# Kernel optimization log

Measured on AMD Instinct MI355X. Metric: run time of the kernel, lower is better.

Reference implementation:

```python
import jax, jax.numpy as jnp
import numpy as np

B, D, L = 8, 512, 2000          # batch, encoder_out_dim, seq_len
E = 300                          # embedding_dim
N1, N2 = 118, 8929               # hierarchy level sizes


def setup_inputs() -> dict:
    key = jax.random.key(0)
    k = jax.random.split(key, 6)
    H = jax.random.normal(k[0], (B, D, L), dtype=jnp.float32)
    Q1w = jax.random.normal(k[1], (N1, E), dtype=jnp.float32) * 0.05   # cat_embedding_matrix
    Q2w = jax.random.normal(k[2], (N2, E), dtype=jnp.float32) * 0.05   # label_embedding_matrix
    # Q12: xavier_uniform over [N2, N1]
    bound = float(np.sqrt(6.0 / (N1 + N2)))
    Q12w = jax.random.uniform(k[3], (N2, N1), minval=-bound, maxval=bound, dtype=jnp.float32)
    # 1x1 conv mapping: weight [D, E], bias [D] (kernel_size=1 squeezed)
    cbound = float(np.sqrt(1.0 / E))
    Wmap = jax.random.uniform(k[4], (D, E), minval=-cbound, maxval=cbound, dtype=jnp.float32)
    bmap = jax.random.uniform(k[5], (D,), minval=-cbound, maxval=cbound, dtype=jnp.float32)
    return {"H": H, "Q1w": Q1w, "Q2w": Q2w, "Q12w": Q12w, "Wmap": Wmap, "bmap": bmap}


def reference(H, Q1w, Q2w, Q12w, Wmap, bmap):
    # 1x1 conv mapping == affine map over embedding dim: [n, E] @ [E, D] + b
    Q1 = Q1w @ Wmap.T + bmap                      # [N1, D]
    E1 = jnp.einsum('nd,bdl->bnl', Q1, H)         # level-1 scores [B, N1, L]
    A1 = jax.nn.softmax(E1, axis=2)
    C1 = jnp.einsum('bnl,bdl->bnd', A1, H)        # [B, N1, D]
    C1 = jnp.einsum('mn,bnd->bmd', Q12w, C1)      # project to level 2: [B, N2, D]
    Q2 = (Q2w @ Wmap.T + bmap) * C1               # [N2, D] * [B, N2, D]
    E2 = jnp.einsum('bmd,bdl->bml', Q2, H)        # level-2 scores [B, N2, L]
    A2 = jax.nn.softmax(E2, axis=2)
    C2 = jnp.einsum('bml,bdl->bmd', A2, H)        # [B, N2, D]
    return (C2, A2)
```

## Files before the change

kernel.cpp:

```cpp
#include <hip/hip_runtime.h>

typedef short    bf16x8 __attribute__((ext_vector_type(8)));
typedef float    f32x4  __attribute__((ext_vector_type(4)));
typedef unsigned short u16x8 __attribute__((ext_vector_type(8)));

__device__ __forceinline__ unsigned short f2bf(float f) {
    unsigned u = __float_as_uint(f);
    return (unsigned short)((u + 0x7fffu + ((u >> 16) & 1u)) >> 16);
}
__device__ __forceinline__ float bf2f(unsigned short h) {
    return __uint_as_float((unsigned)h << 16);
}

template<bool> struct otype            { using T = float; };
template<>     struct otype<true>      { using T = unsigned short; };

template<int BM,int BN,int TM,int TN,bool BT,bool VA,bool VB,bool OB>
__launch_bounds__(256)
__global__ void gemm_f32(const float* __restrict__ A, int lda, long long sA,
                         const float* __restrict__ B, int ldb, long long sB,
                         void* __restrict__ Cv, int ldc, long long sC,
                         int M, int N, int K,
                         const float* __restrict__ bias,
                         const float* __restrict__ mul, int mulld)
{
    constexpr int BK  = 16;
    constexpr int GSA = BM*4/TM;
    constexpr int GSB = BN*4/TN;
    __shared__ float As[BK][BM+4];
    __shared__ float Bs[BK][BN+4];

    const int bz = blockIdx.z;
    A += (long long)bz * sA;
    B += (long long)bz * sB;
    using OT = typename otype<OB>::T;
    OT* C = (OT*)Cv + (long long)bz * sC;
    const int m0 = blockIdx.y * BM;
    const int n0 = blockIdx.x * BN;
    const int tid = threadIdx.x;
    const int tm = tid >> 4;
    const int tn = tid & 15;

    float acc[TM][TN];
#pragma unroll
    for (int i=0;i<TM;++i)
#pragma unroll
        for (int j=0;j<TN;++j) acc[i][j]=0.f;

    for (int k0=0;k0<K;k0+=BK) {
        if constexpr (VA) {
#pragma unroll
            for (int r=0;r<BM*BK/1024;++r) {
                int v = tid + r*256;
                int m = v >> 2, k4 = (v & 3)*4;
                int gm = m0+m, gk = k0+k4;
                float4 val = make_float4(0.f,0.f,0.f,0.f);
                if (gm < M) {
                    if (gk+3 < K) {
                        val = *reinterpret_cast<const float4*>(A + (long long)gm*lda + gk);
                    } else {
                        float t0 = (gk   < K) ? A[(long long)gm*lda+gk  ] : 0.f;
                        float t1 = (gk+1 < K) ? A[(long long)gm*lda+gk+1] : 0.f;
                        float t2 = (gk+2 < K) ? A[(long long)gm*lda+gk+2] : 0.f;
                        val = make_float4(t0,t1,t2,0.f);
                    }
                }
                As[k4+0][m]=val.x; As[k4+1][m]=val.y; As[k4+2][m]=val.z; As[k4+3][m]=val.w;
            }
        } else {
#pragma unroll
            for (int r=0;r<BM*BK/256;++r) {
                int e = tid + r*256;
                int m = e >> 4, k = e & 15;
                int gm=m0+m, gk=k0+k;
                As[k][m] = (gm<M && gk<K) ? A[(long long)gm*lda+gk] : 0.f;
            }
        }
        if constexpr (!BT) {
            if constexpr (VB) {
#pragma unroll
                for (int r=0;r<BK*BN/1024;++r) {
                    int v = tid + r*256;
                    int k = v / (BN/4), n4 = (v % (BN/4))*4;
                    int gk=k0+k, gn=n0+n4;
                    float4 val = make_float4(0.f,0.f,0.f,0.f);
                    if (gk < K) {
                        if (gn+3 < N) {
                            val = *reinterpret_cast<const float4*>(B + (long long)gk*ldb + gn);
                        } else {
                            float t0=(gn  <N)?B[(long long)gk*ldb+gn  ]:0.f;
                            float t1=(gn+1<N)?B[(long long)gk*ldb+gn+1]:0.f;
                            float t2=(gn+2<N)?B[(long long)gk*ldb+gn+2]:0.f;
                            val = make_float4(t0,t1,t2,0.f);
                        }
                    }
                    Bs[k][n4+0]=val.x; Bs[k][n4+1]=val.y; Bs[k][n4+2]=val.z; Bs[k][n4+3]=val.w;
                }
            } else {
#pragma unroll
                for (int r=0;r<BK*BN/256;++r) {
                    int e = tid + r*256;
                    int k = e / BN, n = e % BN;
                    int gk=k0+k, gn=n0+n;
                    Bs[k][n] = (gk<K && gn<N) ? B[(long long)gk*ldb+gn] : 0.f;
                }
            }
        } else {
            if constexpr (VB) {
#pragma unroll
                for (int r=0;r<BN*BK/1024;++r) {
                    int v = tid + r*256;
                    int n = v >> 2, k4 = (v&3)*4;
                    int gn=n0+n, gk=k0+k4;
                    float4 val = make_float4(0.f,0.f,0.f,0.f);
                    if (gn < N) {
                        if (gk+3 < K) {
                            val = *reinterpret_cast<const float4*>(B + (long long)gn*ldb + gk);
                        } else {
                            float t0=(gk  <K)?B[(long long)gn*ldb+gk  ]:0.f;
                            float t1=(gk+1<K)?B[(long long)gn*ldb+gk+1]:0.f;
                            float t2=(gk+2<K)?B[(long long)gn*ldb+gk+2]:0.f;
                            val=make_float4(t0,t1,t2,0.f);
                        }
                    }
                    Bs[k4+0][n]=val.x; Bs[k4+1][n]=val.y; Bs[k4+2][n]=val.z; Bs[k4+3][n]=val.w;
                }
            } else {
#pragma unroll
                for (int r=0;r<BN*BK/256;++r) {
                    int e = tid + r*256;
                    int n = e >> 4, k = e & 15;
                    int gn=n0+n, gk=k0+k;
                    Bs[k][n] = (gn<N && gk<K) ? B[(long long)gn*ldb+gk] : 0.f;
                }
            }
        }
        __syncthreads();
#pragma unroll
        for (int kk=0;kk<BK;++kk) {
            float a[TM], bb[TN];
#pragma unroll
            for (int g=0;g<TM/4;++g) {
                float4 t = *reinterpret_cast<const float4*>(&As[kk][g*GSA + tm*4]);
                a[4*g+0]=t.x; a[4*g+1]=t.y; a[4*g+2]=t.z; a[4*g+3]=t.w;
            }
#pragma unroll
            for (int g=0;g<TN/4;++g) {
                float4 t = *reinterpret_cast<const float4*>(&Bs[kk][g*GSB + tn*4]);
                bb[4*g+0]=t.x; bb[4*g+1]=t.y; bb[4*g+2]=t.z; bb[4*g+3]=t.w;
            }
#pragma unroll
            for (int i=0;i<TM;++i)
#pragma unroll
                for (int j=0;j<TN;++j)
                    acc[i][j] = fmaf(a[i], bb[j], acc[i][j]);
        }
        __syncthreads();
    }
#pragma unroll
    for (int i=0;i<TM;++i) {
        int row = m0 + (i>>2)*GSA + tm*4 + (i&3);
        if (row < M) {
#pragma unroll
            for (int j=0;j<TN;++j) {
                int col = n0 + (j>>2)*GSB + tn*4 + (j&3);
                if (col < N) {
                    float val = acc[i][j];
                    if (bias) val += bias[col];
                    if (mul)  val *= mul[(long long)row*mulld + col];
                    if constexpr (OB) C[(long long)row*ldc + col] = f2bf(val);
                    else              C[(long long)row*ldc + col] = val;
                }
            }
        }
    }
}

template<unsigned F>
__launch_bounds__(512, 4)
__global__ void gemm_mfma_p(const unsigned short* __restrict__ A, int lda, long long sA,
                            const unsigned short* __restrict__ Bt, int ldb, long long sB,
                            void* __restrict__ Cv, int ldc, long long sC,
                            int M, int Ncols, int NX, int NY, int NT,
                            const float* __restrict__ bias,
                            const float* __restrict__ mul, int ldm,
                            float* __restrict__ partial, long long pstride,
                            const float* __restrict__ hsum,
                            const float* __restrict__ invs,
                            float* __restrict__ a2out,
                            float* __restrict__ dump)
{
    __shared__ unsigned short lds[3][12288];

    const int nwg = gridDim.x;
    const int q = nwg >> 3, r = nwg & 7;
    const int xcd = blockIdx.x & 7, idx = blockIdx.x >> 3;
    const int wg = (xcd < r ? xcd*(q+1) : r*(q+1) + (xcd-r)*q) + idx;
    const int nx = wg % NX;
    const int t1 = wg / NX;
    const int my = t1 % NY;
    const int bz = t1 / NY;

    const int tid  = threadIdx.x;
    const int lane = tid & 63, wid = tid >> 6;
    const int wr = wid >> 2, wc = wid & 3;
    const int fr = lane & 15, fq = lane >> 4;
    const int m0 = my * 128;
    const int n0 = nx * 256;

    A  += (long long)bz * sA;
    Bt += (long long)bz * sB;

    const int srow = tid >> 2;
    const int scz  = (tid & 3) ^ ((srow >> 1) & 3);
    long long arow = m0 + srow; if (arow > M-1) arow = M-1;
    const unsigned short* aSrc  = A  + arow*lda + scz*8;
    const unsigned short* bSrc0 = Bt + (long long)(n0 + srow)*ldb + scz*8;
    const unsigned short* bSrc1 = bSrc0 + 128ll*ldb;

    bool wrblk = false, a2ok = false;
    float invv = 0.f;
    float* a2p = nullptr;
    if constexpr ((F & 64) != 0) {
        wrblk = (nx == 0);
        if (wrblk) {
            const int rrow = m0 + srow;
            a2ok = rrow < M;
            const long long ridx = (long long)bz*M + (a2ok ? rrow : M-1);
            invv = invs[ridx];
            asm volatile("" : "+v"(invv));
            a2p = a2out + ridx*2000ll;
        }
    }

    int aoff[4], boff[4];
#pragma unroll
    for (int m=0;m<4;++m) {
        const int ra = wr*64 + m*16 + fr;
        aoff[m] = ra*64 + ((fq ^ ((ra>>1)&3))*16);
    }
#pragma unroll
    for (int n=0;n<4;++n) {
        const int rb = wc*64 + n*16 + fr;
        boff[n] = 8192 + rb*64 + ((fq ^ ((rb>>1)&3))*16);
    }

    f32x4 acc[4][4];
#pragma unroll
    for (int i=0;i<4;++i)
#pragma unroll
        for (int j=0;j<4;++j) acc[i][j] = (f32x4)(0.f);

    auto stage = [&](int s, int t) {
        const int koff = t*32;
        char* base = (char*)&lds[s][0];
        __builtin_amdgcn_global_load_lds(
            (const __attribute__((address_space(1))) void*)(aSrc + koff),
            (__attribute__((address_space(3))) void*)(base + tid*16), 16, 0, 0);
        __builtin_amdgcn_global_load_lds(
            (const __attribute__((address_space(1))) void*)(bSrc0 + koff),
            (__attribute__((address_space(3))) void*)(base + 8192 + tid*16), 16, 0, 0);
        __builtin_amdgcn_global_load_lds(
            (const __attribute__((address_space(1))) void*)(bSrc1 + koff),
            (__attribute__((address_space(3))) void*)(base + 16384 + tid*16), 16, 0, 0);
    };

    stage(0, 0);
    stage(1, NT > 1 ? 1 : 0);
    asm volatile("s_waitcnt vmcnt(3)" ::: "memory");
    __builtin_amdgcn_s_barrier();

    int cur = 0, stg = 2;
    for (int kt = 0; kt < NT; ++kt) {
        int tnx = kt + 2; if (tnx > NT-1) tnx = NT-1;
        stage(stg, tnx);
        const char* bp = (const char*)&lds[cur][0];
        bf16x8 a[4], b[4];
#pragma unroll
        for (int m=0;m<4;++m) a[m] = *(const bf16x8*)(bp + aoff[m]);
#pragma unroll
        for (int n=0;n<4;++n) b[n] = *(const bf16x8*)(bp + boff[n]);
        __builtin_amdgcn_s_setprio(1);
#pragma unroll
        for (int m=0;m<4;++m)
#pragma unroll
            for (int n=0;n<4;++n)
                acc[m][n] = __builtin_amdgcn_mfma_f32_16x16x32_bf16(a[m], b[n], acc[m][n], 0, 0, 0);
        __builtin_amdgcn_s_setprio(0);
        if constexpr ((F & 64) != 0) {
            if (wrblk) {
                u16x8 av = *(const u16x8*)(bp + (tid << 4));
                const int col0 = kt*32 + scz*8;
                const bool ok = a2ok && (col0 < 2000);
                float* p0 = ok ? (a2p + col0) : (dump + (tid << 3));
                float4 o0, o1;
                o0.x = fmaf(bf2f((unsigned short)av[0]), invv, invv);
                o0.y = fmaf(bf2f((unsigned short)av[1]), invv, invv);
                o0.z = fmaf(bf2f((unsigned short)av[2]), invv, invv);
                o0.w = fmaf(bf2f((unsigned short)av[3]), invv, invv);
                o1.x = fmaf(bf2f((unsigned short)av[4]), invv, invv);
                o1.y = fmaf(bf2f((unsigned short)av[5]), invv, invv);
                o1.z = fmaf(bf2f((unsigned short)av[6]), invv, invv);
                o1.w = fmaf(bf2f((unsigned short)av[7]), invv, invv);
                *(float4*)(p0    ) = o0;
                *(float4*)(p0 + 4) = o1;
            }
        }
        asm volatile("s_waitcnt lgkmcnt(0)" ::: "memory");
        if constexpr ((F & 64) != 0) {
            if (wrblk) asm volatile("s_waitcnt vmcnt(5)" ::: "memory");
            else       asm volatile("s_waitcnt vmcnt(3)" ::: "memory");
        } else {
            asm volatile("s_waitcnt vmcnt(3)" ::: "memory");
        }
        __builtin_amdgcn_s_barrier();
        cur = (cur == 2) ? 0 : cur + 1;
        stg = (stg == 2) ? 0 : stg + 1;
    }

    if constexpr ((F & 16) != 0) {
        asm volatile("s_waitcnt vmcnt(0)" ::: "memory");
        __builtin_amdgcn_s_barrier();
        unsigned short* ep = (unsigned short*)&lds[0][0];
        unsigned short* Cb = (unsigned short*)Cv + (long long)bz * sC;
#pragma unroll
        for (int m=0;m<4;++m) {
            const int rl = wr*64 + m*16 + fq*4;
#pragma unroll
            for (int n=0;n<4;++n) {
                const int cl = wc*64 + n*16 + fr;
                const int cb = cl*2;
#pragma unroll
                for (int j=0;j<4;++j) {
                    const int row = rl + j;
                    float x = __expf(acc[m][n][j]) - 1.0f;
                    const int ch = (cb>>5) ^ ((row>>2)&3);
                    *(unsigned short*)((char*)ep + row*512 + (ch<<5) + (cb&31)) = f2bf(x);
                }
            }
        }
        __syncthreads();
        const int rq = tid >> 3;
        const int cq = tid & 7;
#pragma unroll
        for (int half=0; half<2; ++half) {
            const int row = rq + half*64;
            const int grow = m0 + row;
            float s = 0.f;
#pragma unroll
            for (int win=0; win<4; ++win) {
                const int cb = cq*16 + win*128;
                const int ch = (cb>>5) ^ ((row>>2)&3);
                u16x8 v = *(const u16x8*)((const char*)ep + row*512 + (ch<<5) + (cb&31));
#pragma unroll
                for (int i=0;i<8;++i) s += bf2f((unsigned short)v[i]);
                if (grow < M) *(u16x8*)(Cb + (long long)grow*ldc + n0 + (cb>>1)) = v;
            }
            s += __shfl_xor(s, 1); s += __shfl_xor(s, 2); s += __shfl_xor(s, 4);
            if (cq == 0 && grow < M)
                partial[(long long)nx*pstride + (long long)bz*M + grow] = s;
        }
    } else if constexpr ((F & 8) != 0) {
        unsigned short* Ct = (unsigned short*)Cv + (long long)bz * sC;
#pragma unroll
        for (int m=0;m<4;++m) {
            const int rb = m0 + wr*64 + m*16 + fq*4;
#pragma unroll
            for (int n=0;n<4;++n) {
                const int col = n0 + wc*64 + n*16 + fr;
                if (col < Ncols) {
                    float hv = 0.f;
                    if constexpr ((F & 32) != 0) hv = hsum[(long long)bz*Ncols + col];
#pragma unroll
                    for (int j=0;j<4;++j) {
                        const int row = rb + j;
                        float val = 0.f;
                        if (row < M) {
                            val = acc[m][n][j];
                            if constexpr ((F & 32) != 0) val = (val + hv) * invs[(long long)bz*M + row];
                        }
                        Ct[(long long)col*ldc + row] = f2bf(val);
                    }
                }
            }
        }
    } else if constexpr ((F & 4) != 0) {
        asm volatile("s_waitcnt vmcnt(0)" ::: "memory");
        __builtin_amdgcn_s_barrier();
        unsigned short* ep = (unsigned short*)&lds[0][0];
        unsigned short* Cb = (unsigned short*)Cv + (long long)bz * sC;
#pragma unroll
        for (int m=0;m<4;++m) {
            const int rl = wr*64 + m*16 + fq*4;
#pragma unroll
            for (int n=0;n<4;++n) {
                const int cl = wc*64 + n*16 + fr;
                const int gcol = n0 + cl;
                const int cb = cl*2;
                float bv = 0.f;
                if constexpr ((F & 1) != 0) bv = bias[gcol];
#pragma unroll
                for (int j=0;j<4;++j) {
                    const int row = rl + j;
                    float val = acc[m][n][j];
                    if constexpr ((F & 1) != 0) val += bv;
                    if constexpr ((F & 128) != 0) {
                        int mr = m0 + row; if (mr > M-1) mr = M-1;
                        val *= bf2f(((const unsigned short*)mul)[(long long)mr*ldm + gcol]);
                    }
                    if constexpr ((F & 2) != 0) {
                        int mr = m0 + row; if (mr > M-1) mr = M-1;
                        val *= mul[(long long)mr*ldm + gcol];
                    }
                    const int ch = (cb>>5) ^ ((row>>2)&3);
                    *(unsigned short*)((char*)ep + row*512 + (ch<<5) + (cb&31)) = f2bf(val);
                }
            }
        }
        __syncthreads();
        const int rq = tid >> 3;
        const int cq = tid & 7;
#pragma unroll
        for (int half=0; half<2; ++half) {
            const int row = rq + half*64;
            const int grow = m0 + row;
#pragma unroll
            for (int win=0; win<4; ++win) {
                const int cb = cq*16 + win*128;
                const int ch = (cb>>5) ^ ((row>>2)&3);
                u16x8 v = *(const u16x8*)((const char*)ep + row*512 + (ch<<5) + (cb&31));
                const int gc = n0 + (cb>>1);
                if (grow < M && gc < Ncols) *(u16x8*)(Cb + (long long)grow*ldc + gc) = v;
            }
        }
    } else {
        float* Cf = (float*)Cv + (long long)bz * sC;
#pragma unroll
        for (int m=0;m<4;++m) {
            const int rb = m0 + wr*64 + m*16 + fq*4;
#pragma unroll
            for (int n=0;n<4;++n) {
                const int col = n0 + wc*64 + n*16 + fr;
                if (col < Ncols) {
                    float bv = 0.f, hv = 0.f;
                    if constexpr ((F & 1) != 0) bv = bias[col];
                    if constexpr ((F & 32) != 0) hv = hsum[(long long)bz*Ncols + col];
#pragma unroll
                    for (int j=0;j<4;++j) {
                        const int row = rb + j;
                        if (row < M) {
                            float val = acc[m][n][j];
                            if constexpr ((F & 1)   != 0) val += bv;
                            if constexpr ((F & 2)   != 0) val *= mul[(long long)row*ldm + col];
                            if constexpr ((F & 128) != 0) val *= bf2f(((const unsigned short*)mul)[(long long)row*ldm + col]);
                            if constexpr ((F & 32)  != 0) val = (val + hv) * invs[(long long)bz*M + row];
                            Cf[(long long)row*ldc + col] = val;
                        }
                    }
                }
            }
        }
    }
}

template<bool AF32>
__launch_bounds__(512, 2)
__global__ void gemm_mfma(const void* __restrict__ Ain, int lda, long long sA,
                          const unsigned short* __restrict__ Bt, int ldb, long long sB,
                          float* __restrict__ C, int ldc, long long sC,
                          int M, int N, int K, int NT)
{
    __shared__ unsigned short As[2][128*32];
    __shared__ unsigned short Bs[2][256*32];

    const int tid  = threadIdx.x;
    const int lane = tid & 63, wid = tid >> 6;
    const int wr = wid >> 2, wc = wid & 3;
    const int fr = lane & 15, fq = lane >> 4;
    const int bz = blockIdx.z;
    const int m0 = blockIdx.y * 128;
    const int n0 = blockIdx.x * 256;

    const unsigned short* Ab = nullptr;
    const float*          Af = nullptr;
    if constexpr (AF32) Af = (const float*)Ain + (long long)bz * sA;
    else                Ab = (const unsigned short*)Ain + (long long)bz * sA;
    Bt += (long long)bz * sB;
    C  += (long long)bz * sC;

    const int srow = tid >> 2;
    const int sc   = tid & 3;
    const int scz  = sc ^ ((srow >> 1) & 3);
    int arow = m0 + srow; if (arow > M-1) arow = M-1;
    const bool am_ok = (m0 + srow) < M;
    const long long brow0 = n0 + srow;
    const long long brow1 = n0 + 128 + srow;
    const int ldsA  = wid << 10;
    const int ldsB0 = wid << 10;
    const int ldsB1 = 8192 + (wid << 10);

    f32x4 acc[4][4];
#pragma unroll
    for (int i=0;i<4;++i)
#pragma unroll
        for (int j=0;j<4;++j) acc[i][j] = (f32x4)(0.f);

    auto stage = [&](int buf, int t) {
        const long long koff = (long long)t * 32;
        __builtin_amdgcn_global_load_lds(
            (const __attribute__((address_space(1))) void*)(Bt + brow0*ldb + koff + scz*8),
            (__attribute__((address_space(3))) void*)((char*)&Bs[buf][0] + ldsB0), 16, 0, 0);
        __builtin_amdgcn_global_load_lds(
            (const __attribute__((address_space(1))) void*)(Bt + brow1*ldb + koff + scz*8),
            (__attribute__((address_space(3))) void*)((char*)&Bs[buf][0] + ldsB1), 16, 0, 0);
        if constexpr (!AF32) {
            __builtin_amdgcn_global_load_lds(
                (const __attribute__((address_space(1))) void*)(Ab + (long long)arow*lda + koff + scz*8),
                (__attribute__((address_space(3))) void*)((char*)&As[buf][0] + ldsA), 16, 0, 0);
        } else {
            const float* src = Af + (long long)arow*lda + koff + scz*8;
            const int kk = t*32 + scz*8;
            float4 z = make_float4(0.f,0.f,0.f,0.f);
            float4 v0 = (am_ok && kk   < K) ? *(const float4*)(src  ) : z;
            float4 v1 = (am_ok && kk+4 < K) ? *(const float4*)(src+4) : z;
            u16x8 o;
            o[0]=f2bf(v0.x); o[1]=f2bf(v0.y); o[2]=f2bf(v0.z); o[3]=f2bf(v0.w);
            o[4]=f2bf(v1.x); o[5]=f2bf(v1.y); o[6]=f2bf(v1.z); o[7]=f2bf(v1.w);
            *(u16x8*)((char*)&As[buf][0] + tid*16) = o;
        }
    };

    stage(0, 0);
    int cur = 0;
    for (int t = 0; t < NT; ++t) {
        __syncthreads();
        if (t + 1 < NT) stage(cur ^ 1, t + 1);
        const unsigned short* as = As[cur];
        const unsigned short* bs = Bs[cur];
        bf16x8 a[4], b[4];
#pragma unroll
        for (int m=0;m<4;++m) {
            const int ra = wr*64 + m*16 + fr;
            a[m] = *(const bf16x8*)(as + ra*32 + (fq ^ ((ra>>1)&3))*8);
        }
#pragma unroll
        for (int n=0;n<4;++n) {
            const int rb = wc*64 + n*16 + fr;
            b[n] = *(const bf16x8*)(bs + rb*32 + (fq ^ ((rb>>1)&3))*8);
        }
        __builtin_amdgcn_s_setprio(1);
#pragma unroll
        for (int m=0;m<4;++m)
#pragma unroll
            for (int n=0;n<4;++n)
                acc[m][n] = __builtin_amdgcn_mfma_f32_16x16x32_bf16(a[m], b[n], acc[m][n], 0, 0, 0);
        __builtin_amdgcn_s_setprio(0);
        cur ^= 1;
    }
#pragma unroll
    for (int m=0;m<4;++m) {
        const int rb = m0 + wr*64 + m*16 + fq*4;
#pragma unroll
        for (int n=0;n<4;++n) {
            const int col = n0 + wc*64 + n*16 + fr;
            if (col < N) {
#pragma unroll
                for (int j=0;j<4;++j) {
                    const int row = rb + j;
                    if (row < M) C[(long long)row*ldc + col] = acc[m][n][j];
                }
            }
        }
    }
}

__global__ __launch_bounds__(256) void mega_prep(const float* __restrict__ H,
                                                 unsigned short* __restrict__ Hb,
                                                 unsigned short* __restrict__ Htb,
                                                 float* __restrict__ hpart,
                                                 const float* __restrict__ Wmap,  unsigned short* __restrict__ Wb,
                                                 const float* __restrict__ Q1w,   unsigned short* __restrict__ Q1wb,
                                                 const float* __restrict__ Q2w,   unsigned short* __restrict__ Q2wb,
                                                 const float* __restrict__ Q12w,  unsigned short* __restrict__ Q12wb)
{
    __shared__ unsigned short T[64][80];
    const int tid = threadIdx.x;
    int id = blockIdx.x;
    if (id < 2048) {
        const int lt = id & 31;
        const int dt = (id >> 5) & 7;
        const int bz = id >> 8;
        const int d0 = dt * 64;
        const int l0 = lt * 64;
        const float* Hsrc = H + ((long long)bz*512 + d0) * 2000;
        const int dl = tid >> 2;
        const int lc = (tid & 3) * 16;
        float4 v[4];
        float s = 0.f;
#pragma unroll
        for (int i=0;i<4;++i) {
            const int gl = l0 + lc + i*4;
            v[i] = make_float4(0.f,0.f,0.f,0.f);
            if (gl < 2000) v[i] = *(const float4*)(Hsrc + (long long)dl*2000 + gl);
            s += (v[i].x + v[i].y) + (v[i].z + v[i].w);
            T[lc+i*4+0][dl] = f2bf(v[i].x);
            T[lc+i*4+1][dl] = f2bf(v[i].y);
            T[lc+i*4+2][dl] = f2bf(v[i].z);
            T[lc+i*4+3][dl] = f2bf(v[i].w);
        }
        {
            unsigned short* hb = Hb + ((long long)bz*512 + d0 + dl)*2048 + l0 + lc;
            u16x8 h0, h1;
            h0[0]=f2bf(v[0].x); h0[1]=f2bf(v[0].y); h0[2]=f2bf(v[0].z); h0[3]=f2bf(v[0].w);
            h0[4]=f2bf(v[1].x); h0[5]=f2bf(v[1].y); h0[6]=f2bf(v[1].z); h0[7]=f2bf(v[1].w);
            h1[0]=f2bf(v[2].x); h1[1]=f2bf(v[2].y); h1[2]=f2bf(v[2].z); h1[3]=f2bf(v[2].w);
            h1[4]=f2bf(v[3].x); h1[5]=f2bf(v[3].y); h1[6]=f2bf(v[3].z); h1[7]=f2bf(v[3].w);
            *(u16x8*)(hb    ) = h0;
            *(u16x8*)(hb + 8) = h1;
        }
        s += __shfl_xor(s, 1);
        s += __shfl_xor(s, 2);
        if ((tid & 3) == 0)
            hpart[(long long)lt*4096 + bz*512 + d0 + dl] = s;
        __syncthreads();
        unsigned short* Hdst = Htb + ((long long)bz*2048 + l0) * 512 + d0;
        const int ll = tid >> 2;
        const int dc = (tid & 3) * 16;
        u16x8 w0 = *(const u16x8*)&T[ll][dc];
        u16x8 w1 = *(const u16x8*)&T[ll][dc+8];
        *(u16x8*)(Hdst + (long long)ll*512 + dc    ) = w0;
        *(u16x8*)(Hdst + (long long)ll*512 + dc + 8) = w1;
        return;
    }
    id -= 2048;
    if (id < 640) {
        const int i = id*256 + tid;
        if (i < 512*320) {
            const int r2 = i/320, c = i - r2*320;
            Wb[i] = (c < 300) ? f2bf(Wmap[r2*300 + c]) : (unsigned short)0;
        }
    } else if (id < 788) {
        const int i = (id-640)*256 + tid;
        if (i < 118*320) {
            const int r2 = i/320, c = i - r2*320;
            Q1wb[i] = (c < 300) ? f2bf(Q1w[r2*300 + c]) : (unsigned short)0;
        }
    } else if (id < 11950) {
        const int i = (id-788)*256 + tid;
        if (i < 8929*320) {
            const int r2 = i/320, c = i - r2*320;
            Q2wb[i] = (c < 300) ? f2bf(Q2w[r2*300 + c]) : (unsigned short)0;
        }
    } else {
        const int i = (id-11950)*256 + tid;
        if (i < 8929*128) {
            const int r2 = i >> 7, c = i & 127;
            Q12wb[i] = (c < 118) ? f2bf(Q12w[r2*118 + c]) : (unsigned short)0;
        }
    }
}

__global__ __launch_bounds__(256) void reduce_hsum(const float* __restrict__ hpart,
                                                   float* __restrict__ Hsum)
{
    const int r = blockIdx.x*256 + threadIdx.x;
    float s = 0.f;
#pragma unroll
    for (int i=0;i<32;++i) s += hpart[(long long)i*4096 + r];
    Hsum[r] = s;
}

__global__ __launch_bounds__(256) void invs_k(const float* __restrict__ partial,
                                              long long pstride,
                                              float* __restrict__ invs, int n)
{
    const int r = blockIdx.x*256 + threadIdx.x;
    if (r < n) {
        float s = 0.f;
#pragma unroll
        for (int i=0;i<8;++i) s += partial[i*pstride + r];
        invs[r] = 1.0f / (2000.0f + s);
    }
}

__global__ __launch_bounds__(256) void cvt_pad_bf16(const float* __restrict__ H,
                                                    unsigned short* __restrict__ Hb)
{
    const long long idx = (long long)blockIdx.x * 256 + threadIdx.x;
    const long long row = idx >> 8;
    const int l0 = (int)(idx & 255) * 8;
    u16x8 o = (u16x8)(unsigned short)0;
    if (l0 + 8 <= 2000) {
        const float* s = H + row*2000 + l0;
        float4 v0 = *(const float4*)(s);
        float4 v1 = *(const float4*)(s+4);
        o[0]=f2bf(v0.x); o[1]=f2bf(v0.y); o[2]=f2bf(v0.z); o[3]=f2bf(v0.w);
        o[4]=f2bf(v1.x); o[5]=f2bf(v1.y); o[6]=f2bf(v1.z); o[7]=f2bf(v1.w);
    }
    *(u16x8*)(Hb + row*2048 + l0) = o;
}

__global__ __launch_bounds__(256) void cvt_transpose_bf16(const float* __restrict__ H,
                                                          unsigned short* __restrict__ Ht)
{
    __shared__ unsigned short T[64][80];
    const int bz = blockIdx.z;
    const int d0 = blockIdx.y * 64;
    const int l0 = blockIdx.x * 64;
    const float* Hsrc = H + ((long long)bz*512 + d0) * 2000;
    unsigned short* Hdst = Ht + ((long long)bz*2048 + l0) * 512 + d0;
    const int tid = threadIdx.x;
    const int dl = tid >> 2;
    const int lc = (tid & 3) * 16;
#pragma unroll
    for (int i=0;i<4;++i) {
        const int l = lc + i*4;
        const int gl = l0 + l;
        float4 v = make_float4(0.f,0.f,0.f,0.f);
        if (gl < 2000) v = *(const float4*)(Hsrc + (long long)dl*2000 + gl);
        T[l+0][dl] = f2bf(v.x);
        T[l+1][dl] = f2bf(v.y);
        T[l+2][dl] = f2bf(v.z);
        T[l+3][dl] = f2bf(v.w);
    }
    __syncthreads();
    const int ll = tid >> 2;
    const int dc = (tid & 3) * 16;
    u16x8 w0 = *(const u16x8*)&T[ll][dc];
    u16x8 w1 = *(const u16x8*)&T[ll][dc+8];
    *(u16x8*)(Hdst + (long long)ll*512 + dc    ) = w0;
    *(u16x8*)(Hdst + (long long)ll*512 + dc + 8) = w1;
}

__global__ __launch_bounds__(256) void softmax_rows(float* __restrict__ X, int L,
                                                    unsigned short* __restrict__ Xb, int Lb)
{
    const long long row = blockIdx.x;
    float* x = X + row * (long long)L;
    const int tid = threadIdx.x;
    const int nv = L >> 2;
    const bool h0 = tid < nv;
    const bool h1 = tid + 256 < nv;
    float4 t0 = make_float4(0.f,0.f,0.f,0.f);
    float4 t1 = make_float4(0.f,0.f,0.f,0.f);
    float mx = -3.402823e38f;
    if (h0) { t0 = *reinterpret_cast<const float4*>(x + 4*tid);
              mx = fmaxf(fmaxf(t0.x,t0.y), fmaxf(t0.z,t0.w)); }
    if (h1) { t1 = *reinterpret_cast<const float4*>(x + 4*(tid+256));
              mx = fmaxf(mx, fmaxf(fmaxf(t1.x,t1.y), fmaxf(t1.z,t1.w))); }
    __shared__ float sred[4];
#pragma unroll
    for (int o=32;o;o>>=1) mx = fmaxf(mx, __shfl_xor(mx, o));
    if ((tid & 63)==0) sred[tid>>6] = mx;
    __syncthreads();
    mx = fmaxf(fmaxf(sred[0],sred[1]), fmaxf(sred[2],sred[3]));
    __syncthreads();
    float s = 0.f;
    if (h0) {
        t0.x=__expf(t0.x-mx); t0.y=__expf(t0.y-mx); t0.z=__expf(t0.z-mx); t0.w=__expf(t0.w-mx);
        s += (t0.x+t0.y)+(t0.z+t0.w);
    }
    if (h1) {
        t1.x=__expf(t1.x-mx); t1.y=__expf(t1.y-mx); t1.z=__expf(t1.z-mx); t1.w=__expf(t1.w-mx);
        s += (t1.x+t1.y)+(t1.z+t1.w);
    }
#pragma unroll
    for (int o=32;o;o>>=1) s += __shfl_xor(s, o);
    if ((tid & 63)==0) sred[tid>>6] = s;
    __syncthreads();
    s = (sred[0]+sred[1])+(sred[2]+sred[3]);
    const float inv = 1.0f / s;
    if (h0) { t0.x*=inv; t0.y*=inv; t0.z*=inv; t0.w*=inv;
              *reinterpret_cast<float4*>(x + 4*tid) = t0; }
    if (h1) { t1.x*=inv; t1.y*=inv; t1.z*=inv; t1.w*=inv;
              *reinterpret_cast<float4*>(x + 4*(tid+256)) = t1; }
    if (Xb) {
        unsigned short* xb = Xb + row * (long long)Lb;
        if (h0) {
            ushort4 o; o.x=f2bf(t0.x); o.y=f2bf(t0.y); o.z=f2bf(t0.z); o.w=f2bf(t0.w);
            *reinterpret_cast<ushort4*>(xb + 4*tid) = o;
        }
        if (h1) {
            ushort4 o; o.x=f2bf(t1.x); o.y=f2bf(t1.y); o.z=f2bf(t1.z); o.w=f2bf(t1.w);
            *reinterpret_cast<ushort4*>(xb + 4*(tid+256)) = o;
        }
        if (tid < (Lb - L)/4) {
            ushort4 z; z.x=z.y=z.z=z.w=0;
            *reinterpret_cast<ushort4*>(xb + L + 4*tid) = z;
        }
    }
}

extern "C" void kernel_launch(void* const* d_in, const int* in_sizes, int n_in,
                              void* d_out, int out_size, void* d_ws, size_t ws_size,
                              hipStream_t stream)
{
    const float* H    = (const float*)d_in[0];
    const float* Q1w  = (const float*)d_in[1];
    const float* Q2w  = (const float*)d_in[2];
    const float* Q12w = (const float*)d_in[3];
    const float* Wmap = (const float*)d_in[4];
    const float* bmap = (const float*)d_in[5];

    constexpr long long B=8, D=512, L=2000, N1=118, N2=8929;
    constexpr long long C2E = B*N2*D;
    float* out = (float*)d_out;
    float* C2  = out;
    float* A2  = out + C2E;

    dim3 blk(256);

    size_t off = 0;
    auto alloc = [&](size_t n)->size_t { off = (off + 255) & ~(size_t)255; size_t o = off; off += n; return o; };
    const size_t oHb    = alloc(8ll*512*2048*2);
    const size_t oHtb   = alloc(8ll*2048*512*2);
    const size_t oWb    = alloc(512ll*320*2);
    const size_t oQ1wb  = alloc(118ll*320*2);
    const size_t oQ2wb  = alloc(8929ll*320*2);
    const size_t oQ12wb = alloc(8929ll*128*2);
    const size_t oQ1b   = alloc(118ll*512*2);
    const size_t oEmbb  = alloc(8929ll*512*2);
    const size_t oE1x   = alloc(8ll*128*2048*2);
    const size_t oC1tb  = alloc(8ll*512*128*2);
    const size_t oQ2b   = alloc(8ll*8929*512*2);
    const size_t oA2b   = alloc(8ll*8929*2048*2);
    const size_t oPart  = alloc(8ll*8*8929*4);
    const size_t oPart1 = alloc(8ll*944*4);
    const size_t oInvs  = alloc(8ll*8929*4);
    const size_t oInvs1 = alloc(944ll*4);
    const size_t oHsum  = alloc(8ll*512*4);
    const size_t oHpart = alloc(32ll*4096*4);
    const size_t FULL_NEED = off;

    char* ws = (char*)d_ws;

    if (ws_size >= FULL_NEED) {
        unsigned short* Hb    = (unsigned short*)(ws + oHb);
        unsigned short* Htb   = (unsigned short*)(ws + oHtb);
        unsigned short* Wb    = (unsigned short*)(ws + oWb);
        unsigned short* Q1wb  = (unsigned short*)(ws + oQ1wb);
        unsigned short* Q2wb  = (unsigned short*)(ws + oQ2wb);
        unsigned short* Q12wb = (unsigned short*)(ws + oQ12wb);
        unsigned short* Q1b   = (unsigned short*)(ws + oQ1b);
        unsigned short* Embb  = (unsigned short*)(ws + oEmbb);
        unsigned short* E1x   = (unsigned short*)(ws + oE1x);
        unsigned short* C1tb  = (unsigned short*)(ws + oC1tb);
        unsigned short* Q2b   = (unsigned short*)(ws + oQ2b);
        unsigned short* A2b   = (unsigned short*)(ws + oA2b);
        float*          part  = (float*)(ws + oPart);
        float*          part1 = (float*)(ws + oPart1);
        float*          invs  = (float*)(ws + oInvs);
        float*          invs1 = (float*)(ws + oInvs1);
        float*          Hsum  = (float*)(ws + oHsum);
        float*          hpart = (float*)(ws + oHpart);

        mega_prep<<<dim3(18464), blk, 0, stream>>>(H, Hb, Htb, hpart,
                                                   Wmap, Wb, Q1w, Q1wb, Q2w, Q2wb, Q12w, Q12wb);
        reduce_hsum<<<dim3(16), blk, 0, stream>>>(hpart, Hsum);

        gemm_mfma_p<5><<<dim3(2), dim3(512), 0, stream>>>(
            Q1wb, 320, 0, Wb, 320, 0, Q1b, 512, 0, 118, 512, 2, 1, 10,
            bmap, nullptr, 0, nullptr, 0, nullptr, nullptr, nullptr, nullptr);
        gemm_mfma_p<5><<<dim3(140), dim3(512), 0, stream>>>(
            Q2wb, 320, 0, Wb, 320, 0, Embb, 512, 0, 8929, 512, 2, 70, 10,
            bmap, nullptr, 0, nullptr, 0, nullptr, nullptr, nullptr, nullptr);
        gemm_mfma_p<16><<<dim3(64), dim3(512), 0, stream>>>(
            Q1b, 512, 0, Htb, 512, 2048*512, E1x, 2048, 128*2048, 118, 2048, 8, 1, 16,
            nullptr, nullptr, 0, part1, 944, nullptr, nullptr, nullptr, nullptr);
        invs_k<<<dim3(4), blk, 0, stream>>>(part1, 944, invs1, 944);
        gemm_mfma_p<40><<<dim3(16), dim3(512), 0, stream>>>(
            E1x, 2048, 128*2048, Hb, 2048, 512*2048, C1tb, 128, 512*128, 118, 512, 2, 1, 64,
            nullptr, nullptr, 0, nullptr, 0, Hsum, invs1, nullptr, nullptr);
        gemm_mfma_p<132><<<dim3(1120), dim3(512), 0, stream>>>(
            Q12wb, 128, 0, C1tb, 128, 512*128, Q2b, 512, N2*D, 8929, 512, 2, 70, 4,
            nullptr, (const float*)Embb, 512, nullptr, 0, nullptr, nullptr, nullptr, nullptr);
        gemm_mfma_p<16><<<dim3(4480), dim3(512), 0, stream>>>(
            Q2b, 512, N2*D, Htb, 512, 2048*512, A2b, 2048, N2*2048, 8929, 2048, 8, 70, 16,
            nullptr, nullptr, 0, part, 8ll*8929, nullptr, nullptr, nullptr, nullptr);
        invs_k<<<dim3(280), blk, 0, stream>>>(part, 8ll*8929, invs, (int)(B*N2));
        gemm_mfma_p<96><<<dim3(1120), dim3(512), 0, stream>>>(
            A2b, 2048, N2*2048, Hb, 2048, 512*2048, C2, 512, N2*D, 8929, 512, 2, 70, 64,
            nullptr, nullptr, 0, nullptr, 0, Hsum, invs, A2, part);
        return;
    }

    float* Q1  = A2;
    float* emb = Q1  + N1*D;
    float* E1  = emb + N2*D;
    float* C1  = E1  + B*N1*L;

    gemm_f32<64,64,4,4,true,true,true,false><<<dim3(8,2,1), blk, 0, stream>>>(
        Q1w, 300, 0, Wmap, 300, 0, Q1, 512, 0, (int)N1, (int)D, 300, bmap, nullptr, 0);
    gemm_f32<64,64,4,4,true,true,true,false><<<dim3(8,140,1), blk, 0, stream>>>(
        Q2w, 300, 0, Wmap, 300, 0, emb, 512, 0, (int)N2, (int)D, 300, bmap, nullptr, 0);
    gemm_f32<64,64,4,4,false,true,true,false><<<dim3(32,2,8), blk, 0, stream>>>(
        Q1, 512, 0, H, 2000, D*L, E1, 2000, N1*L, (int)N1, (int)L, (int)D, nullptr, nullptr, 0);
    softmax_rows<<<dim3((unsigned)(B*N1)), blk, 0, stream>>>(E1, (int)L, nullptr, 0);
    gemm_f32<64,64,4,4,true,true,true,false><<<dim3(8,2,8), blk, 0, stream>>>(
        E1, 2000, N1*L, H, 2000, D*L, C1, 512, N1*D, (int)N1, (int)D, (int)L, nullptr, nullptr, 0);

    constexpr long long HBE = 8ll*512*2048;
    if (ws_size >= (size_t)(2*HBE*sizeof(unsigned short))) {
        unsigned short* Hb  = (unsigned short*)d_ws;
        unsigned short* Htb = Hb + HBE;
        cvt_pad_bf16<<<dim3(4096), blk, 0, stream>>>(H, Hb);
        cvt_transpose_bf16<<<dim3(32,8,8), blk, 0, stream>>>(H, Htb);
        unsigned short* Q2b = (unsigned short*)C2;
        gemm_f32<64,64,4,4,false,false,true,true><<<dim3(8,140,8), blk, 0, stream>>>(
            Q12w, 118, 0, C1, 512, N1*D, Q2b, 512, N2*D, (int)N2, (int)D, (int)N1, nullptr, emb, 512);
        gemm_mfma_p<0><<<dim3(4480), dim3(512), 0, stream>>>(
            Q2b, 512, N2*D, Htb, 512, 2048*512, A2, 2000, N2*L, (int)N2, (int)L, 8, 70, 16,
            nullptr, nullptr, 0, nullptr, 0, nullptr, nullptr, nullptr, nullptr);
        softmax_rows<<<dim3((unsigned)(B*N2)), blk, 0, stream>>>(A2, (int)L, nullptr, 0);
        gemm_mfma<true><<<dim3(2,70,8), dim3(512), 0, stream>>>(
            A2, 2000, N2*L, Hb, 2048, 512*2048, C2, 512, N2*D,
            (int)N2, (int)D, 2000, 63);
    } else {
        float* Q2 = C2;
        gemm_f32<64,64,4,4,false,false,true,false><<<dim3(8,140,8), blk, 0, stream>>>(
            Q12w, 118, 0, C1, 512, N1*D, Q2, 512, N2*D, (int)N2, (int)D, (int)N1, nullptr, emb, 512);
        gemm_f32<128,128,8,8,false,true,true,false><<<dim3(16,70,8), blk, 0, stream>>>(
            Q2, 512, N2*D, H, 2000, D*L, A2, 2000, N2*L, (int)N2, (int)L, (int)D, nullptr, nullptr, 0);
        softmax_rows<<<dim3((unsigned)(B*N2)), blk, 0, stream>>>(A2, (int)L, nullptr, 0);
        gemm_f32<128,128,8,8,true,true,true,false><<<dim3(4,70,8), blk, 0, stream>>>(
            A2, 2000, N2*L, H, 2000, D*L, C2, 512, N2*D, (int)N2, (int)D, (int)L, nullptr, nullptr, 0);
    }
}
```

Before: 732.8 us.

## Add dedicated triple-buffered MFMA kernel for score GEMMs with exp epilogue

Adds a specialised 256-thread MFMA kernel for the two score GEMMs (E1 and E2). It uses 256x128 tiles, three-stage global-to-LDS async loads, swizzled LDS, XCD-aware workgroup remapping and s_setprio around the MFMA block. The epilogue computes exp-1, stores bf16 through a swizzled LDS staging buffer as coalesced vectors, and writes per-row partial sums over 16 column tiles. The invs reduction now takes a variable partial count. This roughly doubles the partial buffer and the reduction work, and the different tile shape changes occupancy.

```diff
diff --git a/kernel.cpp b/kernel.cpp
--- a/kernel.cpp
+++ b/kernel.cpp
@@ -460,6 +460,152 @@
                 }
             }
         }
+    }
+}
+
+__launch_bounds__(256, 2)
+__global__ void gemm_mfma_q(const unsigned short* __restrict__ A, int lda, long long sA,
+                            const unsigned short* __restrict__ Bt, int ldb, long long sB,
+                            unsigned short* __restrict__ Cb0, int ldc, long long sC,
+                            int M, int NX, int NY, int NT,
+                            float* __restrict__ partial, long long pstride)
+{
+    __shared__ unsigned short lds[3][12288];
+
+    const int nwg = gridDim.x;
+    const int q = nwg >> 3, r = nwg & 7;
+    const int xcd = blockIdx.x & 7, idx = blockIdx.x >> 3;
+    const int wg = (xcd < r ? xcd*(q+1) : r*(q+1) + (xcd-r)*q) + idx;
+    const int nx = wg % NX;
+    const int t1 = wg / NX;
+    const int my = t1 % NY;
+    const int bz = t1 / NY;
+
+    const int tid  = threadIdx.x;
+    const int lane = tid & 63, wid = tid >> 6;
+    const int wr = wid >> 1, wcn = wid & 1;
+    const int fr = lane & 15, fq = lane >> 4;
+    const int m0 = my * 256;
+    const int n0 = nx * 128;
+
+    A  += (long long)bz * sA;
+    Bt += (long long)bz * sB;
+
+    const int t64 = tid >> 2;
+    const int scz = (tid & 3) ^ ((tid >> 3) & 3);
+    const unsigned short* aS[4];
+#pragma unroll
+    for (int i=0;i<4;++i) {
+        long long ar = m0 + i*64 + t64; if (ar > M-1) ar = M-1;
+        aS[i] = A + ar*lda + scz*8;
+    }
+    const unsigned short* bS[2];
+#pragma unroll
+    for (int i=0;i<2;++i)
+        bS[i] = Bt + (long long)(n0 + i*64 + t64)*ldb + scz*8;
+
+    int aoff[8], boff[4];
+#pragma unroll
+    for (int m=0;m<8;++m) {
+        const int ra = wr*128 + m*16 + fr;
+        aoff[m] = ra*64 + ((fq ^ ((ra>>1)&3))*16);
+    }
+#pragma unroll
+    for (int n=0;n<4;++n) {
+        const int rb = wcn*64 + n*16 + fr;
+        boff[n] = 16384 + rb*64 + ((fq ^ ((rb>>1)&3))*16);
+    }
+
+    f32x4 acc[8][4];
+#pragma unroll
+    for (int i=0;i<8;++i)
+#pragma unroll
+        for (int j=0;j<4;++j) acc[i][j] = (f32x4)(0.f);
+
+    auto stage = [&](int s, int t) {
+        const int koff = t*32;
+        char* base = (char*)&lds[s][0];
+#pragma unroll
+        for (int i=0;i<4;++i)
+            __builtin_amdgcn_global_load_lds(
+                (const __attribute__((address_space(1))) void*)(aS[i] + koff),
+                (__attribute__((address_space(3))) void*)(base + i*4096 + tid*16), 16, 0, 0);
+#pragma unroll
+        for (int i=0;i<2;++i)
+            __builtin_amdgcn_global_load_lds(
+                (const __attribute__((address_space(1))) void*)(bS[i] + koff),
+                (__attribute__((address_space(3))) void*)(base + 16384 + i*4096 + tid*16), 16, 0, 0);
+    };
+
+    stage(0, 0);
+    stage(1, NT > 1 ? 1 : 0);
+    asm volatile("s_waitcnt vmcnt(6)" ::: "memory");
+    __builtin_amdgcn_s_barrier();
+
+    int cur = 0, stg = 2;
+    for (int kt = 0; kt < NT; ++kt) {
+        int tnx = kt + 2; if (tnx > NT-1) tnx = NT-1;
+        stage(stg, tnx);
+        const char* bp = (const char*)&lds[cur][0];
+        bf16x8 a[8], b[4];
+#pragma unroll
+        for (int m=0;m<8;++m) a[m] = *(const bf16x8*)(bp + aoff[m]);
+#pragma unroll
+        for (int n=0;n<4;++n) b[n] = *(const bf16x8*)(bp + boff[n]);
+        __builtin_amdgcn_s_setprio(1);
+#pragma unroll
+        for (int m=0;m<8;++m)
+#pragma unroll
+            for (int n=0;n<4;++n)
+                acc[m][n] = __builtin_amdgcn_mfma_f32_16x16x32_bf16(a[m], b[n], acc[m][n], 0, 0, 0);
+        __builtin_amdgcn_s_setprio(0);
+        asm volatile("s_waitcnt lgkmcnt(0)" ::: "memory");
+        asm volatile("s_waitcnt vmcnt(6)" ::: "memory");
+        __builtin_amdgcn_s_barrier();
+        cur = (cur == 2) ? 0 : cur + 1;
+        stg = (stg == 2) ? 0 : stg + 1;
+    }
+
+    asm volatile("s_waitcnt vmcnt(0)" ::: "memory");
+    __builtin_amdgcn_s_barrier();
+    unsigned short* ep = (unsigned short*)&lds[0][0];
+    unsigned short* Cb = Cb0 + (long long)bz * sC;
+#pragma unroll
+    for (int m=0;m<8;++m) {
+        const int rl = wr*128 + m*16 + fq*4;
+#pragma unroll
+        for (int n=0;n<4;++n) {
+            const int cl = wcn*64 + n*16 + fr;
+            const int cb = cl*2;
+#pragma unroll
+            for (int j=0;j<4;++j) {
+                const int row = rl + j;
+                float x = __expf(acc[m][n][j]) - 1.0f;
+                const int ch = (cb>>5) ^ ((row>>2)&7);
+                *(unsigned short*)((char*)ep + row*256 + (ch<<5) + (cb&31)) = f2bf(x);
+            }
+        }
+    }
+    __syncthreads();
+    const int rq = tid >> 3;
+    const int cq = tid & 7;
+#pragma unroll
+    for (int pass=0; pass<8; ++pass) {
+        const int row = rq + pass*32;
+        const int grow = m0 + row;
+        float s = 0.f;
+#pragma unroll
+        for (int win=0; win<2; ++win) {
+            const int cb = cq*16 + win*128;
+            const int ch = (cb>>5) ^ ((row>>2)&7);
+            u16x8 v = *(const u16x8*)((const char*)ep + row*256 + (ch<<5) + (cb&31));
+#pragma unroll
+            for (int i=0;i<8;++i) s += bf2f((unsigned short)v[i]);
+            if (grow < M) *(u16x8*)(Cb + (long long)grow*ldc + n0 + (cb>>1)) = v;
+        }
+        s += __shfl_xor(s, 1); s += __shfl_xor(s, 2); s += __shfl_xor(s, 4);
+        if (cq == 0 && grow < M)
+            partial[(long long)nx*pstride + (long long)bz*M + grow] = s;
     }
 }
 
@@ -672,13 +818,12 @@
 
 __global__ __launch_bounds__(256) void invs_k(const float* __restrict__ partial,
                                               long long pstride,
-                                              float* __restrict__ invs, int n)
+                                              float* __restrict__ invs, int n, int cnt)
 {
     const int r = blockIdx.x*256 + threadIdx.x;
     if (r < n) {
         float s = 0.f;
-#pragma unroll
-        for (int i=0;i<8;++i) s += partial[i*pstride + r];
+        for (int i=0;i<cnt;++i) s += partial[i*pstride + r];
         invs[r] = 1.0f / (2000.0f + s);
     }
 }
@@ -824,8 +969,8 @@
     const size_t oC1tb  = alloc(8ll*512*128*2);
     const size_t oQ2b   = alloc(8ll*8929*512*2);
     const size_t oA2b   = alloc(8ll*8929*2048*2);
-    const size_t oPart  = alloc(8ll*8*8929*4);
-    const size_t oPart1 = alloc(8ll*944*4);
+    const size_t oPart  = alloc(16ll*8*8929*4);
+    const size_t oPart1 = alloc(16ll*944*4);
     const size_t oInvs  = alloc(8ll*8929*4);
     const size_t oInvs1 = alloc(944ll*4);
     const size_t oHsum  = alloc(8ll*512*4);
@@ -864,20 +1009,20 @@
         gemm_mfma_p<5><<<dim3(140), dim3(512), 0, stream>>>(
             Q2wb, 320, 0, Wb, 320, 0, Embb, 512, 0, 8929, 512, 2, 70, 10,
             bmap, nullptr, 0, nullptr, 0, nullptr, nullptr, nullptr, nullptr);
-        gemm_mfma_p<16><<<dim3(64), dim3(512), 0, stream>>>(
-            Q1b, 512, 0, Htb, 512, 2048*512, E1x, 2048, 128*2048, 118, 2048, 8, 1, 16,
-            nullptr, nullptr, 0, part1, 944, nullptr, nullptr, nullptr, nullptr);
-        invs_k<<<dim3(4), blk, 0, stream>>>(part1, 944, invs1, 944);
+        gemm_mfma_q<<<dim3(128), dim3(256), 0, stream>>>(
+            Q1b, 512, 0, Htb, 512, 2048*512, E1x, 2048, 128*2048,
+            118, 16, 1, 16, part1, 944);
+        invs_k<<<dim3(4), blk, 0, stream>>>(part1, 944, invs1, 944, 16);
         gemm_mfma_p<40><<<dim3(16), dim3(512), 0, stream>>>(
             E1x, 2048, 128*2048, Hb, 2048, 512*2048, C1tb, 128, 512*128, 118, 512, 2, 1, 64,
             nullptr, nullptr, 0, nullptr, 0, Hsum, invs1, nullptr, nullptr);
         gemm_mfma_p<132><<<dim3(1120), dim3(512), 0, stream>>>(
             Q12wb, 128, 0, C1tb, 128, 512*128, Q2b, 512, N2*D, 8929, 512, 2, 70, 4,
             nullptr, (const float*)Embb, 512, nullptr, 0, nullptr, nullptr, nullptr, nullptr);
-        gemm_mfma_p<16><<<dim3(4480), dim3(512), 0, stream>>>(
-            Q2b, 512, N2*D, Htb, 512, 2048*512, A2b, 2048, N2*2048, 8929, 2048, 8, 70, 16,
-            nullptr, nullptr, 0, part, 8ll*8929, nullptr, nullptr, nullptr, nullptr);
-        invs_k<<<dim3(280), blk, 0, stream>>>(part, 8ll*8929, invs, (int)(B*N2));
+        gemm_mfma_q<<<dim3(4480), dim3(256), 0, stream>>>(
+            Q2b, 512, N2*D, Htb, 512, 2048*512, A2b, 2048, N2*2048,
+            8929, 16, 35, 16, part, 8ll*8929);
+        invs_k<<<dim3(280), blk, 0, stream>>>(part, 8ll*8929, invs, (int)(B*N2), 16);
         gemm_mfma_p<96><<<dim3(1120), dim3(512), 0, stream>>>(
             A2b, 2048, N2*2048, Hb, 2048, 512*2048, C2, 512, N2*D, 8929, 512, 2, 70, 64,
             nullptr, nullptr, 0, nullptr, 0, Hsum, invs, A2, part);
```

New measurement: 761.6 us. 1.04x slower.
